# Performance work log

Hardware: AMD Instinct MI355X
Metric: run time of the kernel (lower is better)

Reference implementation:

```python
import jax, jax.numpy as jnp
import numpy as np

N_NODES = 50000
N_EDGES = 800000
N_GRAPHS = 128
D_IN = 128
D_H = 256
D_L = 256
D_OUT = 32
BN_EPS = 1e-5


def _dense(k, fan_in, fan_out):
    s = 1.0 / np.sqrt(fan_in)
    kw, kb = jax.random.split(k)
    w = jax.random.uniform(kw, (fan_in, fan_out), jnp.float32, -s, s)
    b = jax.random.uniform(kb, (fan_out,), jnp.float32, -s, s)
    return w, b


def setup_inputs() -> dict:
    key = jax.random.key(0)
    ks = jax.random.split(key, 16)
    inp = {
        'x': jax.random.normal(ks[0], (N_NODES, D_IN), jnp.float32),
        'edge_index': jax.random.randint(ks[1], (2, N_EDGES), 0, N_NODES, jnp.int64),
        'batch': jnp.sort(jax.random.randint(ks[2], (N_NODES,), 0, N_GRAPHS, jnp.int64)),
        'lattice': jax.random.normal(ks[3], (N_GRAPHS, 3, 3), jnp.float32),
    }
    # GIN layers: mlp = Linear(in,h) -> ReLU -> Linear(h,h); BatchNorm(h) affine
    dims = [D_IN, D_H, D_H]
    for i in range(3):
        k1, k2 = jax.random.split(ks[4 + i])
        w1, b1 = _dense(k1, dims[i], D_H)
        w2, b2 = _dense(k2, D_H, D_H)
        inp[f'w{i}a'], inp[f'b{i}a'] = w1, b1
        inp[f'w{i}b'], inp[f'b{i}b'] = w2, b2
        inp[f'gamma{i}'] = jnp.ones((D_H,), jnp.float32)
        inp[f'beta{i}'] = jnp.zeros((D_H,), jnp.float32)
    inp['lw1'], inp['lb1'] = _dense(ks[8], 9, D_L)
    inp['lw2'], inp['lb2'] = _dense(ks[9], D_L, D_L)
    inp['fc1w'], inp['fc1b'] = _dense(ks[10], D_H + D_L, D_H)
    inp['fc2w'], inp['fc2b'] = _dense(ks[11], D_H, D_OUT)
    return inp


def _batchnorm(h, gamma, beta):
    mu = jnp.mean(h, axis=0)
    var = jnp.mean(jnp.square(h - mu), axis=0)
    return gamma * (h - mu) * jax.lax.rsqrt(var + BN_EPS) + beta


def _gin_layer(x, src, dst, w1, b1, w2, b2, gamma, beta):
    # GINConv with eps=0: h_i = MLP(x_i + sum_{j->i} x_j)
    agg = jax.ops.segment_sum(x[src], dst, num_segments=N_NODES)
    h = x + agg
    h = jnp.maximum(h @ w1 + b1, 0.0) @ w2 + b2
    return jnp.maximum(_batchnorm(h, gamma, beta), 0.0)  # relu(norm(conv(x)))


def reference(x, edge_index, batch, lattice,
              w0a, b0a, w0b, b0b, gamma0, beta0,
              w1a, b1a, w1b, b1b, gamma1, beta1,
              w2a, b2a, w2b, b2b, gamma2, beta2,
              lw1, lb1, lw2, lb2, fc1w, fc1b, fc2w, fc2b):
    src, dst = edge_index[0], edge_index[1]
    params = [(w0a, b0a, w0b, b0b, gamma0, beta0),
              (w1a, b1a, w1b, b1b, gamma1, beta1),
              (w2a, b2a, w2b, b2b, gamma2, beta2)]
    h = x
    for (wa, ba, wb, bb, g, be) in params:
        h = _gin_layer(h, src, dst, wa, ba, wb, bb, g, be)
    # global mean pool over graphs
    sums = jax.ops.segment_sum(h, batch, num_segments=N_GRAPHS)
    cnts = jax.ops.segment_sum(jnp.ones((N_NODES,), h.dtype), batch, num_segments=N_GRAPHS)
    pooled = sums / jnp.maximum(cnts, 1.0)[:, None]  # [G, D_H]
    # lattice MLP
    lat = lattice.reshape(lattice.shape[0], -1)  # [G, 9]
    lat = jnp.maximum(lat @ lw1 + lb1, 0.0)
    lat = jnp.maximum(lat @ lw2 + lb2, 0.0)
    comb = jnp.concatenate([pooled, lat], axis=1)
    comb = jnp.maximum(comb @ fc1w + fc1b, 0.0)
    out = comb @ fc2w + fc2b
    return jnp.tanh(out) * 0.5 + 0.5
```

## Files before the change

kernel.cpp:

```cpp
#include <hip/hip_runtime.h>
#include <hip/hip_bf16.h>

#define NN 50000
#define NE 800000
#define NG 128
#define CAP 64

typedef __attribute__((ext_vector_type(4))) float f32x4;
typedef __attribute__((ext_vector_type(8))) short bf16x8;
typedef __attribute__((ext_vector_type(4))) short short4v;
typedef __attribute__((ext_vector_type(2))) short short2v;

__device__ __forceinline__ float bf2f(unsigned short u) {
    union { unsigned int i; float f; } c; c.i = ((unsigned int)u) << 16; return c.f;
}
__device__ __forceinline__ unsigned short f2bf(float f) {
    __hip_bfloat16 b = __float2bfloat16(f);
    return *reinterpret_cast<unsigned short*>(&b);
}

template<int V> struct VecPick;
template<> struct VecPick<4> { using T = short4v; };
template<> struct VecPick<2> { using T = short2v; };

__global__ __launch_bounds__(256) void zero_deg(int* __restrict__ deg) {
    int i = blockIdx.x * 256 + threadIdx.x;
    if (i < NN) deg[i] = 0;
}

__global__ __launch_bounds__(256) void fill_edges(const int* __restrict__ src,
                                                  const int* __restrict__ dst,
                                                  int* __restrict__ deg,
                                                  int* __restrict__ list) {
    int e = blockIdx.x * 256 + threadIdx.x;
    if (e >= NE) return;
    int d = dst[e], s = src[e];
    if ((unsigned)d >= NN || (unsigned)s >= NN) return;
    int slot = atomicAdd(&deg[d], 1);
    if (slot < CAP) list[d * CAP + slot] = s;
}

__global__ __launch_bounds__(256) void init0(const float* __restrict__ x,
                                             unsigned short* __restrict__ h) {
    int i = blockIdx.x * 256 + threadIdx.x;
    if (i >= NN * 32) return;
    int node = i >> 5, c4 = i & 31;
    f32x4 v = reinterpret_cast<const f32x4*>(x)[i];
    short4v b;
#pragma unroll
    for (int c = 0; c < 4; ++c) b[c] = (short)f2bf(v[c]);
    reinterpret_cast<short4v*>(h)[node * 64 + c4] = b;
}

template<int D>
__global__ __launch_bounds__(256) void aggregate(const int* __restrict__ deg,
                                                 const int* __restrict__ list,
                                                 const unsigned short* __restrict__ h,
                                                 unsigned short* __restrict__ abuf) {
    constexpr int V = D / 64;
    using VT = typename VecPick<V>::T;
    int node = blockIdx.x * 4 + (threadIdx.x >> 6);
    if (node >= NN) return;
    const int l = threadIdx.x & 63;
    int d = deg[node]; d = d < CAP ? d : CAP;
    const int* li = list + node * CAP;
    float acc[V];
    {
        VT t = *reinterpret_cast<const VT*>(h + (size_t)node * 256 + l * V);
#pragma unroll
        for (int c = 0; c < V; ++c) acc[c] = bf2f((unsigned short)t[c]);
    }
    int e = 0;
    for (; e + 4 <= d; e += 4) {
        int s0 = li[e], s1 = li[e + 1], s2 = li[e + 2], s3 = li[e + 3];
        VT h0 = *reinterpret_cast<const VT*>(h + (size_t)s0 * 256 + l * V);
        VT h1 = *reinterpret_cast<const VT*>(h + (size_t)s1 * 256 + l * V);
        VT h2 = *reinterpret_cast<const VT*>(h + (size_t)s2 * 256 + l * V);
        VT h3 = *reinterpret_cast<const VT*>(h + (size_t)s3 * 256 + l * V);
#pragma unroll
        for (int c = 0; c < V; ++c)
            acc[c] += (bf2f((unsigned short)h0[c]) + bf2f((unsigned short)h1[c]))
                    + (bf2f((unsigned short)h2[c]) + bf2f((unsigned short)h3[c]));
    }
    for (; e < d; ++e) {
        int s = li[e];
        VT hv = *reinterpret_cast<const VT*>(h + (size_t)s * 256 + l * V);
#pragma unroll
        for (int c = 0; c < V; ++c) acc[c] += bf2f((unsigned short)hv[c]);
    }
    VT t;
#pragma unroll
    for (int c = 0; c < V; ++c) t[c] = (short)f2bf(acc[c]);
    *reinterpret_cast<VT*>(abuf + (size_t)node * 256 + l * V) = t;
}

template<int K, bool RELU>
__global__ __launch_bounds__(256) void node_gemm(unsigned short* AC,
                                                 const unsigned short* __restrict__ WT,
                                                 const float* __restrict__ bias,
                                                 int M) {
    const int lane = threadIdx.x & 63;
    const int wid  = threadIdx.x >> 6;
    const int row0 = blockIdx.x * 64;
    const int col0 = wid * 64;
    const int r16  = lane & 15;
    const int kg   = lane >> 4;

    __shared__ unsigned short ctile[64][264];

    f32x4 acc[4][4];
#pragma unroll
    for (int m = 0; m < 4; ++m)
#pragma unroll
        for (int n = 0; n < 4; ++n) acc[m][n] = (f32x4)0.0f;

#pragma unroll
    for (int ks = 0; ks < K / 32; ++ks) {
        const int kb = ks * 32 + kg * 8;
        bf16x8 afr[4];
#pragma unroll
        for (int m = 0; m < 4; ++m) {
            int row = row0 + m * 16 + r16;
            row = row < M ? row : M - 1;
            afr[m] = *reinterpret_cast<const bf16x8*>(AC + (size_t)row * 256 + kb);
        }
#pragma unroll
        for (int n = 0; n < 4; ++n) {
            const int col = col0 + n * 16 + r16;
            bf16x8 bfr = *reinterpret_cast<const bf16x8*>(WT + (size_t)col * K + kb);
#pragma unroll
            for (int m = 0; m < 4; ++m)
                acc[m][n] = __builtin_amdgcn_mfma_f32_16x16x32_bf16(afr[m], bfr, acc[m][n], 0, 0, 0);
        }
    }
#pragma unroll
    for (int n = 0; n < 4; ++n) {
        const int col = col0 + n * 16 + r16;
        const float bv = bias[col];
#pragma unroll
        for (int m = 0; m < 4; ++m) {
#pragma unroll
            for (int j = 0; j < 4; ++j) {
                int lrow = m * 16 + kg * 4 + j;
                float v = acc[m][n][j] + bv;
                if (RELU) v = fmaxf(v, 0.0f);
                ctile[lrow][col] = f2bf(v);
            }
        }
    }
    __syncthreads();
    const int t = threadIdx.x;
#pragma unroll
    for (int c = t; c < 64 * 32; c += 256) {
        int lrow = c >> 5, cc = (c & 31) * 8;
        int grow = row0 + lrow;
        if (grow < M) {
            bf16x8 v = *reinterpret_cast<const bf16x8*>(&ctile[lrow][cc]);
            *reinterpret_cast<bf16x8*>(AC + (size_t)grow * 256 + cc) = v;
        }
    }
}

#define BN_ROWS_PER_BLOCK 196
__global__ __launch_bounds__(256) void bn_stats(const unsigned short* __restrict__ h,
                                                float* __restrict__ part, int nRows) {
    const int t  = threadIdx.x;
    const int tf = t & 31;
    const int rg = t >> 5;
    const int r0 = blockIdx.x * BN_ROWS_PER_BLOCK;
    const int r1 = min(r0 + BN_ROWS_PER_BLOCK, nRows);
    float s[8], s2[8];
#pragma unroll
    for (int c = 0; c < 8; ++c) { s[c] = 0.f; s2[c] = 0.f; }
    for (int r = r0 + rg; r < r1; r += 8) {
        bf16x8 hv = reinterpret_cast<const bf16x8*>(h + (size_t)r * 256)[tf];
#pragma unroll
        for (int c = 0; c < 8; ++c) {
            float v = bf2f((unsigned short)hv[c]);
            s[c] += v;
            s2[c] = fmaf(v, v, s2[c]);
        }
    }
    __shared__ float redS[8][256];
    __shared__ float redQ[8][256];
#pragma unroll
    for (int c = 0; c < 8; ++c) {
        redS[rg][tf * 8 + c] = s[c];
        redQ[rg][tf * 8 + c] = s2[c];
    }
    __syncthreads();
    float ts = 0.f, tq = 0.f;
#pragma unroll
    for (int g = 0; g < 8; ++g) { ts += redS[g][t]; tq += redQ[g][t]; }
    part[blockIdx.x * 512 + t]       = ts;
    part[blockIdx.x * 512 + 256 + t] = tq;
}

__global__ __launch_bounds__(256) void bn_reduce(const float* __restrict__ part,
                                                 const float* __restrict__ gamma,
                                                 const float* __restrict__ beta,
                                                 float* __restrict__ ss, float invN) {
    const int f = blockIdx.x;
    const int t = threadIdx.x;
    __shared__ float rs[256], rq[256];
    rs[t] = part[t * 512 + f];
    rq[t] = part[t * 512 + 256 + f];
    __syncthreads();
#pragma unroll
    for (int off = 128; off > 0; off >>= 1) {
        if (t < off) { rs[t] += rs[t + off]; rq[t] += rq[t + off]; }
        __syncthreads();
    }
    if (t == 0) {
        float mu  = rs[0] * invN;
        float var = fmaf(-mu, mu, rq[0] * invN);
        float sc  = gamma[f] * rsqrtf(var + 1e-5f);
        ss[f]       = sc;
        ss[256 + f] = fmaf(-sc, mu, beta[f]);
    }
}

__global__ __launch_bounds__(256) void bn_apply(const unsigned short* __restrict__ a,
                                                const float* __restrict__ ss,
                                                unsigned short* __restrict__ h, int n8) {
    int i = blockIdx.x * 256 + threadIdx.x;
    if (i >= n8) return;
    int j = i & 31;
    const f32x4* ssv = reinterpret_cast<const f32x4*>(ss);
    f32x4 sc0 = ssv[2 * j],      sc1 = ssv[2 * j + 1];
    f32x4 sh0 = ssv[64 + 2 * j], sh1 = ssv[64 + 2 * j + 1];
    bf16x8 v = reinterpret_cast<const bf16x8*>(a)[i];
    bf16x8 r;
#pragma unroll
    for (int c = 0; c < 4; ++c)
        r[c] = (short)f2bf(fmaxf(fmaf(bf2f((unsigned short)v[c]), sc0[c], sh0[c]), 0.0f));
#pragma unroll
    for (int c = 0; c < 4; ++c)
        r[4 + c] = (short)f2bf(fmaxf(fmaf(bf2f((unsigned short)v[4 + c]), sc1[c], sh1[c]), 0.0f));
    reinterpret_cast<bf16x8*>(h)[i] = r;
}

__global__ __launch_bounds__(256) void pool_mean(const unsigned short* __restrict__ h,
                                                 const int* __restrict__ batch,
                                                 float* __restrict__ pooled, int nRows) {
    const int g  = blockIdx.x;
    const int t  = threadIdx.x;
    const int tf = t & 31;
    const int rg = t >> 5;
    int lo = 0, hi = nRows;
    while (lo < hi) { int mid = (lo + hi) >> 1; if (batch[mid] < g) lo = mid + 1; else hi = mid; }
    int start = lo;
    hi = nRows;
    while (lo < hi) { int mid = (lo + hi) >> 1; if (batch[mid] < g + 1) lo = mid + 1; else hi = mid; }
    int end = lo;
    float s[8];
#pragma unroll
    for (int c = 0; c < 8; ++c) s[c] = 0.f;
    for (int r = start + rg; r < end; r += 8) {
        bf16x8 hv = reinterpret_cast<const bf16x8*>(h + (size_t)r * 256)[tf];
#pragma unroll
        for (int c = 0; c < 8; ++c) s[c] += bf2f((unsigned short)hv[c]);
    }
    __shared__ float red[8][256];
#pragma unroll
    for (int c = 0; c < 8; ++c) red[rg][tf * 8 + c] = s[c];
    __syncthreads();
    float ts = 0.f;
#pragma unroll
    for (int q = 0; q < 8; ++q) ts += red[q][t];
    pooled[g * 256 + t] = ts / (float)max(end - start, 1);
}

template<int K1, int K2, int N, int ACT>
__global__ void head_gemm(const float* __restrict__ A1, const float* __restrict__ A2,
                          const float* __restrict__ W, const float* __restrict__ bias,
                          float* __restrict__ out) {
    __shared__ float srow[K1 + K2];
    const int g = blockIdx.x, t = threadIdx.x;
    for (int i = t; i < K1; i += blockDim.x) srow[i] = A1[g * K1 + i];
    if (K2 > 0)
        for (int i = t; i < K2; i += blockDim.x) srow[K1 + i] = A2[g * K2 + i];
    __syncthreads();
    if (t < N) {
        float acc = bias[t];
        for (int k = 0; k < K1 + K2; ++k) acc = fmaf(srow[k], W[k * N + t], acc);
        if (ACT == 1) acc = fmaxf(acc, 0.0f);
        if (ACT == 2) acc = tanhf(acc) * 0.5f + 0.5f;
        out[g * N + t] = acc;
    }
}

struct WTParams {
    const float* src[6];
    unsigned short* dst[6];
    int K[6];
};
__global__ void transpose_w(WTParams p) {
    const int w = blockIdx.x;
    const int K = p.K[w];
    const float* s = p.src[w];
    unsigned short* d = p.dst[w];
    const int total = K * 256;
    for (int idx = threadIdx.x; idx < total; idx += blockDim.x) {
        int n = idx / K, k = idx - n * K;
        d[idx] = f2bf(s[k * 256 + n]);
    }
}

extern "C" void kernel_launch(void* const* d_in, const int* in_sizes, int n_in,
                              void* d_out, int out_size, void* d_ws, size_t ws_size,
                              hipStream_t stream) {
    const float* x       = (const float*)d_in[0];
    const int*   ei      = (const int*)d_in[1];
    const int*   batch   = (const int*)d_in[2];
    const float* lattice = (const float*)d_in[3];
    const float* w0a = (const float*)d_in[4],  *b0a = (const float*)d_in[5];
    const float* w0b = (const float*)d_in[6],  *b0b = (const float*)d_in[7];
    const float* g0  = (const float*)d_in[8],  *be0 = (const float*)d_in[9];
    const float* w1a = (const float*)d_in[10], *b1a = (const float*)d_in[11];
    const float* w1b = (const float*)d_in[12], *b1b = (const float*)d_in[13];
    const float* g1  = (const float*)d_in[14], *be1 = (const float*)d_in[15];
    const float* w2a = (const float*)d_in[16], *b2a = (const float*)d_in[17];
    const float* w2b = (const float*)d_in[18], *b2b = (const float*)d_in[19];
    const float* g2  = (const float*)d_in[20], *be2 = (const float*)d_in[21];
    const float* lw1 = (const float*)d_in[22], *lb1 = (const float*)d_in[23];
    const float* lw2 = (const float*)d_in[24], *lb2 = (const float*)d_in[25];
    const float* fc1w= (const float*)d_in[26], *fc1b= (const float*)d_in[27];
    const float* fc2w= (const float*)d_in[28], *fc2b= (const float*)d_in[29];

    const int* srcI = ei;
    const int* dstI = ei + NE;

    char* base = (char*)d_ws;
    size_t used = 0;
    auto alloc = [&](size_t bytes) -> char* {
        char* p = base + used;
        used += (bytes + 255) & ~(size_t)255;
        return p;
    };
    unsigned short* hbuf = (unsigned short*)alloc((size_t)NN * 256 * 2);
    unsigned short* abuf = (unsigned short*)alloc((size_t)NN * 256 * 2);
    int*            list = (int*)alloc((size_t)NN * CAP * 4);
    int*            deg  = (int*)alloc((size_t)NN * 4);
    unsigned short* w0aT = (unsigned short*)alloc(256 * 128 * 2);
    unsigned short* w0bT = (unsigned short*)alloc(256 * 256 * 2);
    unsigned short* w1aT = (unsigned short*)alloc(256 * 256 * 2);
    unsigned short* w1bT = (unsigned short*)alloc(256 * 256 * 2);
    unsigned short* w2aT = (unsigned short*)alloc(256 * 256 * 2);
    unsigned short* w2bT = (unsigned short*)alloc(256 * 256 * 2);
    float* part   = (float*)alloc(256 * 512 * 4);
    float* ss     = (float*)alloc(512 * 4);
    float* pooled = (float*)alloc(128 * 256 * 4);
    float* latb   = (float*)alloc(128 * 256 * 4);
    float* latb2  = (float*)alloc(128 * 256 * 4);
    float* c1     = (float*)alloc(128 * 256 * 4);

    if (used > ws_size) return;

    WTParams tp;
    tp.src[0] = w0a; tp.dst[0] = w0aT; tp.K[0] = 128;
    tp.src[1] = w0b; tp.dst[1] = w0bT; tp.K[1] = 256;
    tp.src[2] = w1a; tp.dst[2] = w1aT; tp.K[2] = 256;
    tp.src[3] = w1b; tp.dst[3] = w1bT; tp.K[3] = 256;
    tp.src[4] = w2a; tp.dst[4] = w2aT; tp.K[4] = 256;
    tp.src[5] = w2b; tp.dst[5] = w2bT; tp.K[5] = 256;
    transpose_w<<<6, 256, 0, stream>>>(tp);

    zero_deg<<<(NN + 255) / 256, 256, 0, stream>>>(deg);
    fill_edges<<<(NE + 255) / 256, 256, 0, stream>>>(srcI, dstI, deg, list);

    const int gemmBlocks = (NN + 63) / 64;
    const int aggBlocks  = (NN + 3) / 4;
    const int n8         = NN * 32;

    init0<<<(NN * 32 + 255) / 256, 256, 0, stream>>>(x, hbuf);
    aggregate<128><<<aggBlocks, 256, 0, stream>>>(deg, list, hbuf, abuf);
    node_gemm<128, true ><<<gemmBlocks, 256, 0, stream>>>(abuf, w0aT, b0a, NN);
    node_gemm<256, false><<<gemmBlocks, 256, 0, stream>>>(abuf, w0bT, b0b, NN);
    bn_stats<<<256, 256, 0, stream>>>(abuf, part, NN);
    bn_reduce<<<256, 256, 0, stream>>>(part, g0, be0, ss, 1.0f / NN);
    bn_apply<<<(n8 + 255) / 256, 256, 0, stream>>>(abuf, ss, hbuf, n8);

    aggregate<256><<<aggBlocks, 256, 0, stream>>>(deg, list, hbuf, abuf);
    node_gemm<256, true ><<<gemmBlocks, 256, 0, stream>>>(abuf, w1aT, b1a, NN);
    node_gemm<256, false><<<gemmBlocks, 256, 0, stream>>>(abuf, w1bT, b1b, NN);
    bn_stats<<<256, 256, 0, stream>>>(abuf, part, NN);
    bn_reduce<<<256, 256, 0, stream>>>(part, g1, be1, ss, 1.0f / NN);
    bn_apply<<<(n8 + 255) / 256, 256, 0, stream>>>(abuf, ss, hbuf, n8);

    aggregate<256><<<aggBlocks, 256, 0, stream>>>(deg, list, hbuf, abuf);
    node_gemm<256, true ><<<gemmBlocks, 256, 0, stream>>>(abuf, w2aT, b2a, NN);
    node_gemm<256, false><<<gemmBlocks, 256, 0, stream>>>(abuf, w2bT, b2b, NN);
    bn_stats<<<256, 256, 0, stream>>>(abuf, part, NN);
    bn_reduce<<<256, 256, 0, stream>>>(part, g2, be2, ss, 1.0f / NN);
    bn_apply<<<(n8 + 255) / 256, 256, 0, stream>>>(abuf, ss, hbuf, n8);

    pool_mean<<<NG, 256, 0, stream>>>(hbuf, batch, pooled, NN);
    head_gemm<9,   0,   256, 1><<<NG, 256, 0, stream>>>(lattice, nullptr, lw1, lb1, latb);
    head_gemm<256, 0,   256, 1><<<NG, 256, 0, stream>>>(latb, nullptr, lw2, lb2, latb2);
    head_gemm<256, 256, 256, 1><<<NG, 256, 0, stream>>>(pooled, latb2, fc1w, fc1b, c1);
    head_gemm<256, 0,   32,  2><<<NG, 64, 0, stream>>>(c1, nullptr, fc2w, fc2b, (float*)d_out);
}
```

Baseline: 698.9 us.

## Fuse two-layer node MLP into one kernel and unroll aggregation by eight

Merges the two per-layer node GEMM launches into a single kernel. The ReLU'd hidden tile stays in shared memory and feeds the second GEMM directly, which removes one global write and read of the 50000x256 intermediate plus one launch per layer. The neighbour aggregation loop also gets an 8-way unrolled path so more gathers are in flight at once. The cost is higher register pressure in both kernels and an extra shared-memory round trip per block.

```diff
diff --git a/kernel.cpp b/kernel.cpp
--- a/kernel.cpp
+++ b/kernel.cpp
@@ -71,16 +71,29 @@
         for (int c = 0; c < V; ++c) acc[c] = bf2f((unsigned short)t[c]);
     }
     int e = 0;
+    for (; e + 8 <= d; e += 8) {
+        VT hv[8];
+#pragma unroll
+        for (int q = 0; q < 8; ++q) {
+            int s = li[e + q];
+            hv[q] = *reinterpret_cast<const VT*>(h + (size_t)s * 256 + l * V);
+        }
+#pragma unroll
+        for (int q = 0; q < 8; ++q)
+#pragma unroll
+            for (int c = 0; c < V; ++c) acc[c] += bf2f((unsigned short)hv[q][c]);
+    }
     for (; e + 4 <= d; e += 4) {
-        int s0 = li[e], s1 = li[e + 1], s2 = li[e + 2], s3 = li[e + 3];
-        VT h0 = *reinterpret_cast<const VT*>(h + (size_t)s0 * 256 + l * V);
-        VT h1 = *reinterpret_cast<const VT*>(h + (size_t)s1 * 256 + l * V);
-        VT h2 = *reinterpret_cast<const VT*>(h + (size_t)s2 * 256 + l * V);
-        VT h3 = *reinterpret_cast<const VT*>(h + (size_t)s3 * 256 + l * V);
-#pragma unroll
-        for (int c = 0; c < V; ++c)
-            acc[c] += (bf2f((unsigned short)h0[c]) + bf2f((unsigned short)h1[c]))
-                    + (bf2f((unsigned short)h2[c]) + bf2f((unsigned short)h3[c]));
+        VT hv[4];
+#pragma unroll
+        for (int q = 0; q < 4; ++q) {
+            int s = li[e + q];
+            hv[q] = *reinterpret_cast<const VT*>(h + (size_t)s * 256 + l * V);
+        }
+#pragma unroll
+        for (int q = 0; q < 4; ++q)
+#pragma unroll
+            for (int c = 0; c < V; ++c) acc[c] += bf2f((unsigned short)hv[q][c]);
     }
     for (; e < d; ++e) {
         int s = li[e];
@@ -94,11 +107,13 @@
     *reinterpret_cast<VT*>(abuf + (size_t)node * 256 + l * V) = t;
 }
 
-template<int K, bool RELU>
-__global__ __launch_bounds__(256) void node_gemm(unsigned short* AC,
-                                                 const unsigned short* __restrict__ WT,
-                                                 const float* __restrict__ bias,
-                                                 int M) {
+template<int K1>
+__global__ __launch_bounds__(256) void node_mlp(unsigned short* AC,
+                                                const unsigned short* __restrict__ W1T,
+                                                const float* __restrict__ b1,
+                                                const unsigned short* __restrict__ W2T,
+                                                const float* __restrict__ b2,
+                                                int M) {
     const int lane = threadIdx.x & 63;
     const int wid  = threadIdx.x >> 6;
     const int row0 = blockIdx.x * 64;
@@ -115,7 +130,7 @@
         for (int n = 0; n < 4; ++n) acc[m][n] = (f32x4)0.0f;
 
 #pragma unroll
-    for (int ks = 0; ks < K / 32; ++ks) {
+    for (int ks = 0; ks < K1 / 32; ++ks) {
         const int kb = ks * 32 + kg * 8;
         bf16x8 afr[4];
 #pragma unroll
@@ -127,7 +142,7 @@
 #pragma unroll
         for (int n = 0; n < 4; ++n) {
             const int col = col0 + n * 16 + r16;
-            bf16x8 bfr = *reinterpret_cast<const bf16x8*>(WT + (size_t)col * K + kb);
+            bf16x8 bfr = *reinterpret_cast<const bf16x8*>(W1T + (size_t)col * K1 + kb);
 #pragma unroll
             for (int m = 0; m < 4; ++m)
                 acc[m][n] = __builtin_amdgcn_mfma_f32_16x16x32_bf16(afr[m], bfr, acc[m][n], 0, 0, 0);
@@ -136,15 +151,49 @@
 #pragma unroll
     for (int n = 0; n < 4; ++n) {
         const int col = col0 + n * 16 + r16;
-        const float bv = bias[col];
+        const float bv = b1[col];
 #pragma unroll
         for (int m = 0; m < 4; ++m) {
 #pragma unroll
             for (int j = 0; j < 4; ++j) {
                 int lrow = m * 16 + kg * 4 + j;
-                float v = acc[m][n][j] + bv;
-                if (RELU) v = fmaxf(v, 0.0f);
-                ctile[lrow][col] = f2bf(v);
+                ctile[lrow][col] = f2bf(fmaxf(acc[m][n][j] + bv, 0.0f));
+            }
+        }
+    }
+    __syncthreads();
+
+#pragma unroll
+    for (int m = 0; m < 4; ++m)
+#pragma unroll
+        for (int n = 0; n < 4; ++n) acc[m][n] = (f32x4)0.0f;
+#pragma unroll
+    for (int ks = 0; ks < 8; ++ks) {
+        const int kb = ks * 32 + kg * 8;
+        bf16x8 afr[4];
+#pragma unroll
+        for (int m = 0; m < 4; ++m)
+            afr[m] = *reinterpret_cast<const bf16x8*>(&ctile[m * 16 + r16][kb]);
+#pragma unroll
+        for (int n = 0; n < 4; ++n) {
+            const int col = col0 + n * 16 + r16;
+            bf16x8 bfr = *reinterpret_cast<const bf16x8*>(W2T + (size_t)col * 256 + kb);
+#pragma unroll
+            for (int m = 0; m < 4; ++m)
+                acc[m][n] = __builtin_amdgcn_mfma_f32_16x16x32_bf16(afr[m], bfr, acc[m][n], 0, 0, 0);
+        }
+    }
+    __syncthreads();
+#pragma unroll
+    for (int n = 0; n < 4; ++n) {
+        const int col = col0 + n * 16 + r16;
+        const float bv = b2[col];
+#pragma unroll
+        for (int m = 0; m < 4; ++m) {
+#pragma unroll
+            for (int j = 0; j < 4; ++j) {
+                int lrow = m * 16 + kg * 4 + j;
+                ctile[lrow][col] = f2bf(acc[m][n][j] + bv);
             }
         }
     }
@@ -375,22 +424,19 @@
 
     init0<<<(NN * 32 + 255) / 256, 256, 0, stream>>>(x, hbuf);
     aggregate<128><<<aggBlocks, 256, 0, stream>>>(deg, list, hbuf, abuf);
-    node_gemm<128, true ><<<gemmBlocks, 256, 0, stream>>>(abuf, w0aT, b0a, NN);
-    node_gemm<256, false><<<gemmBlocks, 256, 0, stream>>>(abuf, w0bT, b0b, NN);
+    node_mlp<128><<<gemmBlocks, 256, 0, stream>>>(abuf, w0aT, b0a, w0bT, b0b, NN);
     bn_stats<<<256, 256, 0, stream>>>(abuf, part, NN);
     bn_reduce<<<256, 256, 0, stream>>>(part, g0, be0, ss, 1.0f / NN);
     bn_apply<<<(n8 + 255) / 256, 256, 0, stream>>>(abuf, ss, hbuf, n8);
 
     aggregate<256><<<aggBlocks, 256, 0, stream>>>(deg, list, hbuf, abuf);
-    node_gemm<256, true ><<<gemmBlocks, 256, 0, stream>>>(abuf, w1aT, b1a, NN);
-    node_gemm<256, false><<<gemmBlocks, 256, 0, stream>>>(abuf, w1bT, b1b, NN);
+    node_mlp<256><<<gemmBlocks, 256, 0, stream>>>(abuf, w1aT, b1a, w1bT, b1b, NN);
     bn_stats<<<256, 256, 0, stream>>>(abuf, part, NN);
     bn_reduce<<<256, 256, 0, stream>>>(part, g1, be1, ss, 1.0f / NN);
     bn_apply<<<(n8 + 255) / 256, 256, 0, stream>>>(abuf, ss, hbuf, n8);
 
     aggregate<256><<<aggBlocks, 256, 0, stream>>>(deg, list, hbuf, abuf);
-    node_gemm<256, true ><<<gemmBlocks, 256, 0, stream>>>(abuf, w2aT, b2a, NN);
-    node_gemm<256, false><<<gemmBlocks, 256, 0, stream>>>(abuf, w2bT, b2b, NN);
+    node_mlp<256><<<gemmBlocks, 256, 0, stream>>>(abuf, w2aT, b2a, w2bT, b2b, NN);
     bn_stats<<<256, 256, 0, stream>>>(abuf, part, NN);
     bn_reduce<<<256, 256, 0, stream>>>(part, g2, be2, ss, 1.0f / NN);
     bn_apply<<<(n8 + 255) / 256, 256, 0, stream>>>(abuf, ss, hbuf, n8);
```

Measured after the change: 651.2 us. 6.8% less time.
